# Kernel tuning notes

Hardware: AMD Instinct MI355X
Metric: run time of the kernel (lower is better)

The kernel has to match this reference:

```python
import jax, jax.numpy as jnp
import numpy as np
import math

B, N, D, H, L, F, K = 4, 256, 768, 32, 12, 3072, 128
HD = D // H
ATOM_TYPES = 64
EDGE_TYPES = ATOM_TYPES * ATOM_TYPES
BLOCKS = 1
SQRT_2PI = math.sqrt(2.0 * math.pi)


def _ln(x, g, b):
    m = jnp.mean(x, -1, keepdims=True)
    v = jnp.mean((x - m) ** 2, -1, keepdims=True)
    return (x - m) * jax.lax.rsqrt(v + 1e-5) * g + b


def _gelu(x):
    return jax.nn.gelu(x, approximate=False)


def setup_inputs():
    key = jax.random.key(0)
    ks = iter(jax.random.split(key, 64))
    def nrm(shape, s=0.02):
        return jax.random.normal(next(ks), shape, jnp.float32) * s
    inp = dict(
        atoms=jax.random.randint(next(ks), (B, N), 0, ATOM_TYPES),
        tags=jax.random.randint(next(ks), (B, N), 0, 3),
        pos=jax.random.normal(next(ks), (B, N, 3), jnp.float32) * 3.0,
        real_mask=jnp.ones((B, N), dtype=bool),
        atom_emb=nrm((ATOM_TYPES, D)),
        tag_emb=nrm((3, D)),
        gbf_means=jax.random.uniform(next(ks), (K,), jnp.float32, 0.0, 3.0),
        gbf_stds=jax.random.uniform(next(ks), (K,), jnp.float32, 0.0, 3.0),
        gbf_mul=jnp.ones((EDGE_TYPES, 1), jnp.float32),
        gbf_bias=jnp.zeros((EDGE_TYPES, 1), jnp.float32),
        bp_w1=nrm((K, K)), bp_b1=jnp.zeros((K,), jnp.float32),
        bp_w2=nrm((H, K)), bp_b2=jnp.zeros((H,), jnp.float32),
        ep_w=nrm((D, K)), ep_b=jnp.zeros((D,), jnp.float32),
        ln1_g=jnp.ones((L, D), jnp.float32), ln1_b=jnp.zeros((L, D), jnp.float32),
        wqkv=nrm((L, 3 * D, D)), bqkv=jnp.zeros((L, 3 * D), jnp.float32),
        wo=nrm((L, D, D)), bo=jnp.zeros((L, D), jnp.float32),
        ln2_g=jnp.ones((L, D), jnp.float32), ln2_b=jnp.zeros((L, D), jnp.float32),
        w1=nrm((L, F, D)), b1=jnp.zeros((L, F), jnp.float32),
        w2=nrm((L, D, F)), b2=jnp.zeros((L, D), jnp.float32),
        fln_g=jnp.ones((D,), jnp.float32), fln_b=jnp.zeros((D,), jnp.float32),
        en_w1=nrm((D, D)), en_b1=jnp.zeros((D,), jnp.float32),
        en_w2=nrm((1, D)), en_b2=jnp.zeros((1,), jnp.float32),
        eagg=nrm((3, 1), 0.01),
        nq_w=nrm((D, D)), nq_b=jnp.zeros((D,), jnp.float32),
        nk_w=nrm((D, D)), nk_b=jnp.zeros((D,), jnp.float32),
        nv_w=nrm((D, D)), nv_b=jnp.zeros((D,), jnp.float32),
        f1_w=nrm((1, D)), f1_b=jnp.zeros((1,), jnp.float32),
        f2_w=nrm((1, D)), f2_b=jnp.zeros((1,), jnp.float32),
        f3_w=nrm((1, D)), f3_b=jnp.zeros((1,), jnp.float32),
    )
    return inp


def _forward(atoms, tags, real_mask, pos, atom_emb, tag_emb, gbf_means, gbf_stds, gbf_mul, gbf_bias,
             bp_w1, bp_b1, bp_w2, bp_b2, ep_w, ep_b,
             ln1_g, ln1_b, wqkv, bqkv, wo, bo, ln2_g, ln2_b, w1, b1, w2, b2,
             fln_g, fln_b, en_w1, en_b1, en_w2, en_b2, eagg,
             nq_w, nq_b, nk_w, nk_b, nv_w, nv_b, f1_w, f1_b, f2_w, f2_b, f3_w, f3_b):
    pad = atoms == 0                                              # [B,N]
    # delta[b,i,j] = pos[b,j] - pos[b,i]  (matches pos.unsqueeze(1) - pos.unsqueeze(2))
    delta = pos[:, None, :, :] - pos[:, :, None, :]               # [B,N,N,3]
    sq = jnp.sum(delta * delta, axis=-1)
    dist = jnp.sqrt(jnp.maximum(sq, 1e-24))                       # safe norm, zero grad on diagonal
    delta = delta / (dist[..., None] + 1e-5)
    edge_type = atoms[:, :, None] * ATOM_TYPES + atoms[:, None, :]  # [B,N,N]
    # Gaussian basis layer
    mul = gbf_mul[edge_type]                                      # [B,N,N,1]
    add = gbf_bias[edge_type]                                     # [B,N,N,1]
    x = mul * dist[..., None] + add                               # [B,N,N,1] -> broadcast to K
    std = jnp.abs(gbf_stds) + 1e-5                                # [K]
    z = (x - gbf_means) / std
    gbf = jnp.exp(-0.5 * z * z) / (SQRT_2PI * std)                # [B,N,N,K]
    edge_feat = jnp.where(pad[:, None, :, None], 0.0, gbf)
    node = tag_emb[tags] + atom_emb[atoms] + (edge_feat.sum(-2) @ ep_w.T + ep_b)  # [B,N,D]
    bias = _gelu(gbf @ bp_w1.T + bp_b1) @ bp_w2.T + bp_b2         # [B,N,N,H]
    bias = jnp.transpose(bias, (0, 3, 1, 2))                      # [B,H,N,N]
    bias = jnp.where(pad[:, None, None, :], -jnp.inf, bias)
    scale = HD ** -0.5
    h = node
    for _ in range(BLOCKS):
        for l in range(L):
            r = h
            y = _ln(h, ln1_g[l], ln1_b[l])
            qkv = y @ wqkv[l].T + bqkv[l]
            q, k, v = jnp.split(qkv, 3, axis=-1)
            q = q.reshape(B, N, H, HD).transpose(0, 2, 1, 3) * scale
            k = k.reshape(B, N, H, HD).transpose(0, 2, 1, 3)
            v = v.reshape(B, N, H, HD).transpose(0, 2, 1, 3)
            a = jnp.einsum('bhid,bhjd->bhij', q, k) + bias
            a = jax.nn.softmax(a, axis=-1)
            o = jnp.einsum('bhij,bhjd->bhid', a, v).transpose(0, 2, 1, 3).reshape(B, N, D)
            h = r + (o @ wo[l].T + bo[l])
            r = h
            y = _ln(h, ln2_g[l], ln2_b[l])
            y = _gelu(y @ w1[l].T + b1[l]) @ w2[l].T + b2[l]
            h = r + y
    out = _ln(h, fln_g, fln_b)                                    # [B,N,D]
    # energy head (eval: no dropout)
    eng = _gelu(out @ en_w1.T + en_b1) @ en_w2.T + en_b2          # [B,N,1]
    eng = (eng * eagg[tags])[..., 0]                              # [B,N]
    omask = (tags > 0) & real_mask
    eng_output = (eng * omask).sum(-1)                            # [B]
    # node task head
    q = (out @ nq_w.T + nq_b).reshape(B, N, H, HD).transpose(0, 2, 1, 3) * scale
    k = (out @ nk_w.T + nk_b).reshape(B, N, H, HD).transpose(0, 2, 1, 3)
    v = (out @ nv_w.T + nv_b).reshape(B, N, H, HD).transpose(0, 2, 1, 3)
    a = jnp.einsum('bhid,bhjd->bhij', q, k) + bias
    a = jax.nn.softmax(a, axis=-1)                                # [B,H,N,N]
    # rot_attn_probs @ v, fused: [b,h,i,j]*[b,i,j,c]*[b,h,j,d] -> [b,i,c,h,d]
    xf = jnp.einsum('bhij,bijc,bhjd->bichd', a, delta, v).reshape(B, N, 3, D)
    f1 = xf[:, :, 0] @ f1_w.T + f1_b
    f2 = xf[:, :, 1] @ f2_w.T + f2_b
    f3 = xf[:, :, 2] @ f3_w.T + f3_b
    node_output = jnp.concatenate([f1, f2, f3], axis=-1)          # [B,N,3]
    return eng_output, node_output, omask[..., None]


def reference(atoms, tags, pos, real_mask, atom_emb, tag_emb, gbf_means, gbf_stds, gbf_mul, gbf_bias,
              bp_w1, bp_b1, bp_w2, bp_b2, ep_w, ep_b,
              ln1_g, ln1_b, wqkv, bqkv, wo, bo, ln2_g, ln2_b, w1, b1, w2, b2,
              fln_g, fln_b, en_w1, en_b1, en_w2, en_b2, eagg,
              nq_w, nq_b, nk_w, nk_b, nv_w, nv_b, f1_w, f1_b, f2_w, f2_b, f3_w, f3_b):
    return _forward(atoms, tags, real_mask, pos, atom_emb, tag_emb, gbf_means, gbf_stds, gbf_mul, gbf_bias,
                    bp_w1, bp_b1, bp_w2, bp_b2, ep_w, ep_b,
                    ln1_g, ln1_b, wqkv, bqkv, wo, bo, ln2_g, ln2_b, w1, b1, w2, b2,
                    fln_g, fln_b, en_w1, en_b1, en_w2, en_b2, eagg,
                    nq_w, nq_b, nk_w, nk_b, nv_w, nv_b, f1_w, f1_b, f2_w, f2_b, f3_w, f3_b)
```

## Files before the change

kernel.cpp:

```cpp
#include <hip/hip_runtime.h>
#include <math.h>

constexpr int B_ = 4, N_ = 256, D_ = 768, H_ = 32, HD_ = 24, L_ = 12, F_ = 3072, K_ = 128;
constexpr float SCALE_ = 0.20412414523193150f;
constexpr float ISQRT2_ = 0.70710678118654752f;

typedef short bf16x8 __attribute__((ext_vector_type(8)));
typedef float f32x4 __attribute__((ext_vector_type(4)));
typedef unsigned short u16x4 __attribute__((ext_vector_type(4)));
typedef unsigned short u16x8 __attribute__((ext_vector_type(8)));
typedef unsigned int u32x4 __attribute__((ext_vector_type(4)));

#define DEV __device__ __forceinline__
#define MFMA16(a, b, c) __builtin_amdgcn_mfma_f32_16x16x32_bf16(a, b, c, 0, 0, 0)

DEV void gload_lds16(const unsigned short* g, unsigned short* l) {
  __builtin_amdgcn_global_load_lds(
      (const __attribute__((address_space(1))) unsigned int*)(g),
      (__attribute__((address_space(3))) unsigned int*)(l), 16, 0, 0);
}

DEV float gelu_f(float x) { return 0.5f * x * (1.0f + erff(x * ISQRT2_)); }

DEV unsigned short f2bf(float f) {
  unsigned u = __float_as_uint(f);
  return (unsigned short)((u + 0x7FFFu + ((u >> 16) & 1u)) >> 16);
}
DEV float bf2f(unsigned short u) { return __uint_as_float(((unsigned)u) << 16); }
DEV unsigned packbf(float a, float b) {
  return (unsigned)f2bf(a) | ((unsigned)f2bf(b) << 16);
}
DEV bf16x8 u4_to_bf8(u32x4 x) { union { u32x4 a; bf16x8 b; } u; u.a = x; return u.b; }

DEV float breduce_sum(float v, float* sred, int tid) {
#pragma unroll
  for (int o = 32; o > 0; o >>= 1) v += __shfl_xor(v, o);
  if ((tid & 63) == 0) sred[tid >> 6] = v;
  __syncthreads();
  v = (sred[0] + sred[1]) + (sred[2] + sred[3]);
  __syncthreads();
  return v;
}

__global__ __launch_bounds__(256) void cast_bias_kernel(
    const float* __restrict__ w1f, const float* __restrict__ w2f,
    unsigned short* __restrict__ d1, unsigned short* __restrict__ d2) {
  const int i = blockIdx.x * 256 + threadIdx.x;
  const float* s;
  unsigned short* d;
  int j;
  if (i < 4096) { s = w1f; d = d1; j = i; }
  else { s = w2f; d = d2; j = i - 4096; }
  const float4 v = ((const float4*)s)[j];
  u16x4 o = {f2bf(v.x), f2bf(v.y), f2bf(v.z), f2bf(v.w)};
  ((u16x4*)d)[j] = o;
}

__global__ __launch_bounds__(256) void castlayer_kernel(
    const float* __restrict__ wqkv, const float* __restrict__ wo,
    const float* __restrict__ w1, const float* __restrict__ w2,
    unsigned short* __restrict__ arena) {
  const unsigned i = blockIdx.x * 256 + threadIdx.x;
  const float* s; unsigned j;
  if (i < 221184u) { s = wqkv; j = i; }
  else if (i < 294912u) { s = wo; j = i - 221184u; }
  else if (i < 589824u) { s = w1; j = i - 294912u; }
  else { s = w2; j = i - 589824u; }
  const float4 a = ((const float4*)s)[2u * j];
  const float4 b = ((const float4*)s)[2u * j + 1u];
  u16x8 o = {f2bf(a.x), f2bf(a.y), f2bf(a.z), f2bf(a.w),
             f2bf(b.x), f2bf(b.y), f2bf(b.z), f2bf(b.w)};
  ((u16x8*)arena)[i] = o;
}

__global__ __launch_bounds__(256) void castheads_kernel(
    const float* __restrict__ a, const float* __restrict__ b,
    const float* __restrict__ c, const float* __restrict__ d,
    unsigned short* __restrict__ arena) {
  const unsigned i = blockIdx.x * 256 + threadIdx.x;
  const unsigned r = i / 73728u;
  const unsigned j = i - r * 73728u;
  const float* s = (r == 0) ? a : (r == 1) ? b : (r == 2) ? c : d;
  const float4 a0 = ((const float4*)s)[2u * j];
  const float4 a1 = ((const float4*)s)[2u * j + 1u];
  u16x8 o = {f2bf(a0.x), f2bf(a0.y), f2bf(a0.z), f2bf(a0.w),
             f2bf(a1.x), f2bf(a1.y), f2bf(a1.z), f2bf(a1.w)};
  ((u16x8*)arena)[i] = o;
}

__global__ __launch_bounds__(256) void edge_pre_kernel(
    const int* __restrict__ atoms, const float* __restrict__ pos,
    const float* __restrict__ gbf_mul, const float* __restrict__ gbf_bias,
    const float* __restrict__ gbf_means, const float* __restrict__ gbf_stds,
    float* __restrict__ deltaw, float* __restrict__ xvalw, float* __restrict__ nsumw)
{
  const int tid = threadIdx.x;
  const int bi = blockIdx.x;
  const int b = bi >> 8;
  __shared__ float spos[3];
  __shared__ float sxv[256];
  __shared__ int   spad[256];
  __shared__ float red[256];
  if (tid < 3) spos[tid] = pos[(size_t)bi * 3 + tid];
  __syncthreads();
  {
    const int j = tid;
    const float px = pos[(size_t)(b * N_ + j) * 3 + 0];
    const float py = pos[(size_t)(b * N_ + j) * 3 + 1];
    const float pz = pos[(size_t)(b * N_ + j) * 3 + 2];
    const float dx = px - spos[0], dy = py - spos[1], dz = pz - spos[2];
    const float sq = dx * dx + dy * dy + dz * dz;
    const float dist = sqrtf(fmaxf(sq, 1e-24f));
    const float inv = 1.f / (dist + 1e-5f);
    const size_t e = (size_t)bi * N_ + j;
    deltaw[e * 3 + 0] = dx * inv;
    deltaw[e * 3 + 1] = dy * inv;
    deltaw[e * 3 + 2] = dz * inv;
    const int et = atoms[bi] * 64 + atoms[b * N_ + j];
    const float xv = gbf_mul[et] * dist + gbf_bias[et];
    xvalw[e] = xv;
    sxv[j] = xv;
    spad[j] = (atoms[b * N_ + j] == 0);
  }
  __syncthreads();
  const int k = tid & 127;
  const float mean = gbf_means[k];
  const float st = fabsf(gbf_stds[k]) + 1e-5f;
  const float istd = 1.f / st;
  const float coef = 0.39894228040143268f * istd;
  float acc = 0.f;
  const int jbase = tid >> 7;
  for (int t = 0; t < 128; ++t) {
    const int j = jbase + (t << 1);
    if (!spad[j]) {
      const float z = (sxv[j] - mean) * istd;
      acc += __expf(-0.5f * z * z) * coef;
    }
  }
  red[tid] = acc;
  __syncthreads();
  if (tid < 128) nsumw[(size_t)bi * K_ + tid] = red[tid] + red[tid + 128];
}

__global__ __launch_bounds__(256) void bias_mfma_kernel(
    const float* __restrict__ xvalw, const int* __restrict__ atoms,
    const float* __restrict__ gbf_means, const float* __restrict__ gbf_stds,
    const unsigned short* __restrict__ w1b, const float* __restrict__ b1,
    const unsigned short* __restrict__ w2b, const float* __restrict__ b2,
    unsigned short* __restrict__ biasb)
{
  __shared__ __align__(16) unsigned short sw1[128 * 128];
  __shared__ __align__(16) unsigned short sw2[32 * 128];
  __shared__ float smean[128], sistd[128], scoef[128], sb1[128], sb2[32];
  const int tid = threadIdx.x;
  const int l = tid & 63;
  const int w = tid >> 6;
  const size_t e0 = (size_t)blockIdx.x * 64;
  const int bB = (int)(e0 >> 16);
  const int iI = (int)((e0 >> 8) & 255);
  const int j0 = (int)(e0 & 255);
  const int lr = l & 15;
  const int lg = l >> 4;

  {
    const int rin = l >> 4;
    const int slot = l & 15;
#pragma unroll
    for (int q = 0; q < 8; ++q) {
      const int rbase = w * 32 + q * 4;
      const int row = rbase + rin;
      const int gs = slot ^ (row & 15);
      gload_lds16(w1b + row * 128 + gs * 8, &sw1[rbase * 128]);
    }
#pragma unroll
    for (int q = 0; q < 2; ++q) {
      const int rbase = w * 8 + q * 4;
      const int row = rbase + rin;
      const int gs = slot ^ (row & 15);
      gload_lds16(w2b + row * 128 + gs * 8, &sw2[rbase * 128]);
    }
  }
  if (tid < 128) {
    const float st = fabsf(gbf_stds[tid]) + 1e-5f;
    const float is = 1.f / st;
    smean[tid] = gbf_means[tid];
    sistd[tid] = is;
    scoef[tid] = 0.39894228040143268f * is;
    sb1[tid] = b1[tid];
  } else if (tid < 160) {
    sb2[tid - 128] = b2[tid - 128];
  }
  const int el = w * 16 + lr;
  const float xv = xvalw[e0 + el];
  const bool padq = (atoms[bB * N_ + j0 + el] == 0);
  __syncthreads();

  bf16x8 bG[4];
#pragma unroll
  for (int ks = 0; ks < 4; ++ks) {
    u16x8 t;
#pragma unroll
    for (int j = 0; j < 8; ++j) {
      const int k = ks * 32 + lg * 8 + j;
      const float z = (xv - smean[k]) * sistd[k];
      t[j] = f2bf(__expf(-0.5f * z * z) * scoef[k]);
    }
    union { u16x8 a; bf16x8 b; } u; u.a = t;
    bG[ks] = u.b;
  }

  f32x4 accM[8];
#pragma unroll
  for (int f = 0; f < 8; ++f) accM[f] = (f32x4)0.f;
#pragma unroll
  for (int ks = 0; ks < 4; ++ks) {
#pragma unroll
    for (int f = 0; f < 8; ++f) {
      const int row = f * 16 + lr;
      const int sl = (ks * 4 + lg) ^ (row & 15);
      const bf16x8 aW = *(const bf16x8*)&sw1[row * 128 + (sl << 3)];
      accM[f] = MFMA16(aW, bG[ks], accM[f]);
    }
  }

  unsigned pm[8][2];
#pragma unroll
  for (int f = 0; f < 8; ++f) {
    float g[4];
#pragma unroll
    for (int r = 0; r < 4; ++r)
      g[r] = gelu_f(accM[f][r] + sb1[f * 16 + lg * 4 + r]);
    pm[f][0] = packbf(g[0], g[1]);
    pm[f][1] = packbf(g[2], g[3]);
  }

  f32x4 accH[2];
  accH[0] = (f32x4)0.f; accH[1] = (f32x4)0.f;
#pragma unroll
  for (int ks = 0; ks < 4; ++ks) {
    const int s0 = ((((lg << 1)) & 3) << 4) + lr;
    const int s1 = ((((lg << 1) + 1) & 3) << 4) + lr;
    const int sel = lg >> 1;
    const unsigned a0 = __shfl(pm[2 * ks][0], s0), b0 = __shfl(pm[2 * ks + 1][0], s0);
    const unsigned a1 = __shfl(pm[2 * ks][1], s0), b1v = __shfl(pm[2 * ks + 1][1], s0);
    const unsigned a2 = __shfl(pm[2 * ks][0], s1), b2v = __shfl(pm[2 * ks + 1][0], s1);
    const unsigned a3 = __shfl(pm[2 * ks][1], s1), b3v = __shfl(pm[2 * ks + 1][1], s1);
    u32x4 bw;
    bw.x = sel ? b0 : a0;
    bw.y = sel ? b1v : a1;
    bw.z = sel ? b2v : a2;
    bw.w = sel ? b3v : a3;
    const bf16x8 bMid = u4_to_bf8(bw);
#pragma unroll
    for (int hf = 0; hf < 2; ++hf) {
      const int row = hf * 16 + lr;
      const int sl = (ks * 4 + lg) ^ (row & 15);
      const bf16x8 aW2 = *(const bf16x8*)&sw2[row * 128 + (sl << 3)];
      accH[hf] = MFMA16(aW2, bMid, accH[hf]);
    }
  }

  const size_t obase = (((size_t)bB * H_) * N_ + iI) * N_ + j0 + el;
#pragma unroll
  for (int hf = 0; hf < 2; ++hf) {
#pragma unroll
    for (int r = 0; r < 4; ++r) {
      const int h = hf * 16 + lg * 4 + r;
      const unsigned short v = padq ? (unsigned short)0xFF80
                                    : f2bf(accH[hf][r] + sb2[h]);
      biasb[obase + (size_t)h * N_ * N_] = v;
    }
  }
}

__global__ __launch_bounds__(256) void node_init_kernel(
    const int* __restrict__ atoms, const int* __restrict__ tags,
    const float* __restrict__ atom_emb, const float* __restrict__ tag_emb,
    const float* __restrict__ nsumw, const float* __restrict__ ep_w,
    const float* __restrict__ ep_b, float* __restrict__ hbuf)
{
  const int bi = blockIdx.x;
  const int tid = threadIdx.x;
  __shared__ float ns[K_];
  if (tid < K_) ns[tid] = nsumw[(size_t)bi * K_ + tid];
  __syncthreads();
  const int at = atoms[bi], tg = tags[bi];
  for (int d = tid; d < D_; d += 256) {
    float acc = tag_emb[tg * D_ + d] + atom_emb[at * D_ + d] + ep_b[d];
    const float* w = ep_w + (size_t)d * K_;
#pragma unroll 8
    for (int kk = 0; kk < K_; ++kk) acc = fmaf(ns[kk], w[kk], acc);
    hbuf[(size_t)bi * D_ + d] = acc;
  }
}

__global__ __launch_bounds__(256) void ln_kernel(
    const float* __restrict__ x, const float* __restrict__ gg,
    const float* __restrict__ bb, unsigned short* __restrict__ y)
{
  const int bi = blockIdx.x;
  const int tid = threadIdx.x;
  __shared__ float sred[4];
  const float* row = x + (size_t)bi * D_;
  const float v0 = row[tid], v1 = row[tid + 256], v2 = row[tid + 512];
  float s = breduce_sum(v0 + v1 + v2, sred, tid);
  const float mean = s * (1.f / 768.f);
  const float d0 = v0 - mean, d1 = v1 - mean, d2 = v2 - mean;
  float q = breduce_sum(d0 * d0 + d1 * d1 + d2 * d2, sred, tid);
  const float inv = rsqrtf(q * (1.f / 768.f) + 1e-5f);
  unsigned short* out = y + (size_t)bi * D_;
  out[tid]       = f2bf(d0 * inv * gg[tid]       + bb[tid]);
  out[tid + 256] = f2bf(d1 * inv * gg[tid + 256] + bb[tid + 256]);
  out[tid + 512] = f2bf(d2 * inv * gg[tid + 512] + bb[tid + 512]);
}

template <int S>
__global__ __launch_bounds__(256) void reduce_ln_kernel(
    const float* __restrict__ P, const float* __restrict__ bias,
    float* __restrict__ hbuf, const float* __restrict__ gg,
    const float* __restrict__ bb, unsigned short* __restrict__ y)
{
  const int row = blockIdx.x;
  const int tid = threadIdx.x;
  __shared__ float sred[4];
  float h[3];
#pragma unroll
  for (int t = 0; t < 3; ++t) {
    const int c = tid + (t << 8);
    float s = bias[c];
#pragma unroll
    for (int z = 0; z < S; ++z)
      s += P[((size_t)z * (B_ * N_) + row) * 768 + c];
    const float hv = hbuf[(size_t)row * 768 + c] + s;
    hbuf[(size_t)row * 768 + c] = hv;
    h[t] = hv;
  }
  float sm = breduce_sum(h[0] + h[1] + h[2], sred, tid);
  const float mean = sm * (1.f / 768.f);
  const float d0 = h[0] - mean, d1 = h[1] - mean, d2 = h[2] - mean;
  float q = breduce_sum(d0 * d0 + d1 * d1 + d2 * d2, sred, tid);
  const float inv = rsqrtf(q * (1.f / 768.f) + 1e-5f);
  unsigned short* out = y + (size_t)row * 768;
  out[tid]       = f2bf(d0 * inv * gg[tid]       + bb[tid]);
  out[tid + 256] = f2bf(d1 * inv * gg[tid + 256] + bb[tid + 256]);
  out[tid + 512] = f2bf(d2 * inv * gg[tid + 512] + bb[tid + 512]);
}

template <int EPI, int OB>
__global__ __launch_bounds__(256) void gemm_mfma(
    const unsigned short* __restrict__ A, const unsigned short* __restrict__ W,
    const float* __restrict__ bias, const float* __restrict__ bias2,
    const float* __restrict__ bias3, const float* __restrict__ bias4,
    float* __restrict__ C, unsigned short* __restrict__ Cb,
    int M, int N, int K, int lda, int ldw)
{
  if (EPI == 4) {
    const int z = blockIdx.z;
    A += (size_t)z * K;
    W += (size_t)z * K;
    C += (size_t)z * M * N;
  }
  __shared__ __align__(16) unsigned short sA[2][64 * 64];
  __shared__ __align__(16) unsigned short sB[2][64 * 64];
  const int tid = threadIdx.x;
  const int l = tid & 63;
  const int w = tid >> 6;
  const int m0 = blockIdx.y * 64;
  const int n0 = blockIdx.x * 64;
  const int wm = w >> 1, wn = w & 1;
  const int lr = l & 15;
  const int lg = l >> 4;
  const int r0 = (w << 4) + (l >> 3);
  const int s0 = (l & 7) ^ (r0 & 7);

  f32x4 acc[2][2];
#pragma unroll
  for (int mi = 0; mi < 2; ++mi)
#pragma unroll
    for (int ni = 0; ni < 2; ++ni) acc[mi][ni] = (f32x4)0.f;

  auto stage = [&](int buf, int t) {
    const size_t kb = (size_t)t << 6;
    unsigned short* lA = &sA[buf][(w << 4) << 6];
    unsigned short* lB = &sB[buf][(w << 4) << 6];
    gload_lds16(A + (size_t)(m0 + r0) * lda + kb + (s0 << 3), lA);
    gload_lds16(A + (size_t)(m0 + r0 + 8) * lda + kb + (s0 << 3), lA + 8 * 64);
    gload_lds16(W + (size_t)(n0 + r0) * ldw + kb + (s0 << 3), lB);
    gload_lds16(W + (size_t)(n0 + r0 + 8) * ldw + kb + (s0 << 3), lB + 8 * 64);
  };

  stage(0, 0);
  const int nt = K >> 6;
  for (int t = 0; t < nt; ++t) {
    __syncthreads();
    if (t + 1 < nt) stage((t + 1) & 1, t + 1);
    const unsigned short* bA = sA[t & 1];
    const unsigned short* bBs = sB[t & 1];
    bf16x8 af[2][2], bfr[2][2];
#pragma unroll
    for (int mi = 0; mi < 2; ++mi) {
      const int row = (wm << 5) + (mi << 4) + lr;
#pragma unroll
      for (int kk = 0; kk < 2; ++kk) {
        const int sl = ((kk << 2) + lg) ^ (row & 7);
        af[mi][kk] = *(const bf16x8*)&bA[(row << 6) + (sl << 3)];
      }
    }
#pragma unroll
    for (int ni = 0; ni < 2; ++ni) {
      const int row = (wn << 5) + (ni << 4) + lr;
#pragma unroll
      for (int kk = 0; kk < 2; ++kk) {
        const int sl = ((kk << 2) + lg) ^ (row & 7);
        bfr[ni][kk] = *(const bf16x8*)&bBs[(row << 6) + (sl << 3)];
      }
    }
#pragma unroll
    for (int kk = 0; kk < 2; ++kk)
#pragma unroll
      for (int mi = 0; mi < 2; ++mi)
#pragma unroll
        for (int ni = 0; ni < 2; ++ni)
          acc[mi][ni] = MFMA16(af[mi][kk], bfr[ni][kk], acc[mi][ni]);
  }

#pragma unroll
  for (int mi = 0; mi < 2; ++mi)
#pragma unroll
    for (int ni = 0; ni < 2; ++ni) {
      const int n = n0 + (wn << 5) + (ni << 4) + lr;
      float bv = 0.f;
      int seg = 0;
      if (EPI == 3) {
        seg = n / 768;
        const float* bp = (seg == 0) ? bias : (seg == 1) ? bias2
                         : (seg == 2) ? bias3 : bias4;
        bv = bp[n - seg * 768];
      } else if (EPI != 4) {
        bv = bias[n];
      }
#pragma unroll
      for (int r = 0; r < 4; ++r) {
        const int m = m0 + (wm << 5) + (mi << 4) + lg * 4 + r;
        float v = acc[mi][ni][r] + bv;
        if (EPI == 1) v = gelu_f(v);
        if (EPI == 3 && seg == 3) v = gelu_f(v);
        if (OB) Cb[(size_t)m * N + n] = f2bf(v);
        else C[(size_t)m * N + n] = v;
      }
    }
}

template <bool PROBS>
__global__ __launch_bounds__(256) void attn_mfma_kernel(
    const unsigned short* __restrict__ Q, const unsigned short* __restrict__ Kp,
    const unsigned short* __restrict__ Vp, const int stride,
    const unsigned short* __restrict__ biasb, unsigned short* __restrict__ obuf,
    unsigned short* __restrict__ aprob,
    const float* __restrict__ f1w, const float* __restrict__ f2w,
    const float* __restrict__ f3w, float* __restrict__ wv)
{
  __shared__ __align__(16) unsigned short sK[256 * 40];
  __shared__ __align__(16) unsigned short sVt[32 * 264];
  __shared__ __align__(16) unsigned short sP[64 * 264];
  const int tid = threadIdx.x;
  const int l = tid & 63, w = tid >> 6;
  const int bh = blockIdx.x, b = bh >> 5, hh = bh & 31;
  const int i0 = blockIdx.y * 64;
  const int lr = l & 15, lg = l >> 4;

#pragma unroll
  for (int it = 0; it < 3; ++it) {
    const int c = tid + (it << 8);
    const int row = c / 3, part = c - row * 3;
    *(u16x8*)&sK[row * 40 + part * 8] =
        *(const u16x8*)&Kp[(size_t)(b * N_ + row) * stride + hh * HD_ + part * 8];
  }
  {
    u16x8 z = {0, 0, 0, 0, 0, 0, 0, 0};
    *(u16x8*)&sK[tid * 40 + 24] = z;
  }
  if (!PROBS) {
    const int j = tid;
    const unsigned short* vr = &Vp[(size_t)(b * N_ + j) * stride + hh * HD_];
    const u16x8 v0 = *(const u16x8*)vr;
    const u16x8 v1 = *(const u16x8*)(vr + 8);
    const u16x8 v2 = *(const u16x8*)(vr + 16);
#pragma unroll
    for (int d = 0; d < 8; ++d) {
      sVt[d * 264 + j] = v0[d];
      sVt[(8 + d) * 264 + j] = v1[d];
      sVt[(16 + d) * 264 + j] = v2[d];
    }
  }
  bf16x8 aQ;
  if (lg < 3) {
    const u16x8 q = *(const u16x8*)&Q[(size_t)(b * N_ + i0 + (w << 4) + lr) * stride + hh * HD_ + lg * 8];
    union { u16x8 a; bf16x8 b; } u; u.a = q;
    aQ = u.b;
  } else {
    bf16x8 t = {0, 0, 0, 0, 0, 0, 0, 0};
    aQ = t;
  }
  __syncthreads();

  f32x4 acc[16];
#pragma unroll
  for (int ni = 0; ni < 16; ++ni) {
    const bf16x8 bK = *(const bf16x8*)&sK[(ni * 16 + lr) * 40 + lg * 8];
    acc[ni] = MFMA16(aQ, bK, (f32x4)0.f);
  }

  float invr[4];
#pragma unroll
  for (int r = 0; r < 4; ++r) {
    const int iloc = (w << 4) + lg * 4 + r;
    const unsigned short* bp =
        &biasb[(((size_t)(b * H_ + hh)) * N_ + i0 + iloc) * N_ + lr];
    float mx = -INFINITY;
#pragma unroll
    for (int ni = 0; ni < 16; ++ni) {
      const float s = acc[ni][r] * SCALE_ + bf2f(bp[ni * 16]);
      acc[ni][r] = s;
      mx = fmaxf(mx, s);
    }
    mx = fmaxf(mx, __shfl_xor(mx, 1));
    mx = fmaxf(mx, __shfl_xor(mx, 2));
    mx = fmaxf(mx, __shfl_xor(mx, 4));
    mx = fmaxf(mx, __shfl_xor(mx, 8));
    float sum = 0.f;
#pragma unroll
    for (int ni = 0; ni < 16; ++ni) {
      const float e = __expf(acc[ni][r] - mx);
      acc[ni][r] = e;
      sum += e;
    }
    sum += __shfl_xor(sum, 1);
    sum += __shfl_xor(sum, 2);
    sum += __shfl_xor(sum, 4);
    sum += __shfl_xor(sum, 8);
    const float inv = 1.f / sum;
    invr[r] = inv;
#pragma unroll
    for (int ni = 0; ni < 16; ++ni)
      sP[iloc * 264 + ni * 16 + lr] = f2bf(PROBS ? acc[ni][r] * inv
                                                 : acc[ni][r]);
  }
  __syncthreads();

  if (PROBS) {
#pragma unroll
    for (int it = 0; it < 8; ++it) {
      const int idx = tid + it * 256;
      const int row = idx >> 5, c = idx & 31;
      *(u16x8*)&aprob[(((size_t)(b * H_ + hh)) * N_ + i0 + row) * N_ + c * 8] =
          *(const u16x8*)&sP[row * 264 + c * 8];
    }
    if (blockIdx.y == 0) {
      const int j = tid;
      const unsigned short* vr = &Vp[(size_t)(b * N_ + j) * stride + hh * HD_];
      const u16x8 v0 = *(const u16x8*)vr;
      const u16x8 v1 = *(const u16x8*)(vr + 8);
      const u16x8 v2 = *(const u16x8*)(vr + 16);
      float s0 = 0.f, s1 = 0.f, s2 = 0.f;
#pragma unroll
      for (int d = 0; d < 8; ++d) {
        const float e0 = bf2f(v0[d]), e1 = bf2f(v1[d]), e2 = bf2f(v2[d]);
        s0 = fmaf(e0, f1w[hh * HD_ + d], s0);
        s0 = fmaf(e1, f1w[hh * HD_ + 8 + d], s0);
        s0 = fmaf(e2, f1w[hh * HD_ + 16 + d], s0);
        s1 = fmaf(e0, f2w[hh * HD_ + d], s1);
        s1 = fmaf(e1, f2w[hh * HD_ + 8 + d], s1);
        s1 = fmaf(e2, f2w[hh * HD_ + 16 + d], s1);
        s2 = fmaf(e0, f3w[hh * HD_ + d], s2);
        s2 = fmaf(e1, f3w[hh * HD_ + 8 + d], s2);
        s2 = fmaf(e2, f3w[hh * HD_ + 16 + d], s2);
      }
      wv[((size_t)(0 * B_ + b) * H_ + hh) * N_ + j] = s0;
      wv[((size_t)(1 * B_ + b) * H_ + hh) * N_ + j] = s1;
      wv[((size_t)(2 * B_ + b) * H_ + hh) * N_ + j] = s2;
    }
  } else {
    f32x4 accO[2];
    accO[0] = (f32x4)0.f; accO[1] = (f32x4)0.f;
#pragma unroll
    for (int ks = 0; ks < 8; ++ks) {
      const bf16x8 aP = *(const bf16x8*)&sP[((w << 4) + lr) * 264 + ks * 32 + lg * 8];
      const bf16x8 bV0 = *(const bf16x8*)&sVt[lr * 264 + ks * 32 + lg * 8];
      const bf16x8 bV1 = *(const bf16x8*)&sVt[(16 + lr) * 264 + ks * 32 + lg * 8];
      accO[0] = MFMA16(aP, bV0, accO[0]);
      accO[1] = MFMA16(aP, bV1, accO[1]);
    }
#pragma unroll
    for (int ni = 0; ni < 2; ++ni) {
      const int n = ni * 16 + lr;
      if (n < HD_) {
#pragma unroll
        for (int r = 0; r < 4; ++r) {
          const int i = i0 + (w << 4) + lg * 4 + r;
          obuf[(size_t)(b * N_ + i) * D_ + hh * HD_ + n] = f2bf(accO[ni][r] * invr[r]);
        }
      }
    }
  }
}

__global__ __launch_bounds__(256) void engnode_kernel(
    const unsigned short* __restrict__ t1, const int stride,
    const float* __restrict__ en_w2, const float* __restrict__ en_b2,
    const float* __restrict__ eagg, const int* __restrict__ tags,
    float* __restrict__ engpn)
{
  const int bi = blockIdx.x;
  const int tid = threadIdx.x;
  __shared__ float sred[4];
  const unsigned short* row = t1 + (size_t)bi * stride;
  float acc = bf2f(row[tid]) * en_w2[tid] + bf2f(row[tid + 256]) * en_w2[tid + 256] +
              bf2f(row[tid + 512]) * en_w2[tid + 512];
  acc = breduce_sum(acc, sred, tid);
  if (tid == 0) {
    const int tg = tags[bi];
    engpn[bi] = (tg > 0) ? (acc + en_b2[0]) * eagg[tg] : 0.f;
  }
}

__global__ __launch_bounds__(256) void engsum_omask_kernel(
    const float* __restrict__ engpn, const int* __restrict__ tags,
    float* __restrict__ out)
{
  const int bid = blockIdx.x;
  const int tid = threadIdx.x;
  if (bid < 4) {
    __shared__ float sred[4];
    float v = breduce_sum(engpn[bid * N_ + tid], sred, tid);
    if (tid == 0) out[bid] = v;
  } else {
    const int idx = (bid - 4) * 256 + tid;
    out[4 + B_ * N_ * 3 + idx] = (tags[idx] > 0) ? 1.f : 0.f;
  }
}

__global__ __launch_bounds__(256) void nodeout_kernel(
    const unsigned short* __restrict__ aprob, const float* __restrict__ wv,
    const float* __restrict__ deltaw, const float* __restrict__ f1b,
    const float* __restrict__ f2b, const float* __restrict__ f3b,
    float* __restrict__ out)
{
  const int bi = blockIdx.x;
  const int tid = threadIdx.x;
  const int b = bi >> 8;
  const int i = bi & 255;
  __shared__ float sred[4];
  const unsigned short* ap = aprob + (((size_t)b * H_) * N_ + i) * N_ + tid;
  const float* wv0 = wv + ((size_t)(0 * B_ + b) * H_) * N_ + tid;
  const float* wv1 = wv + ((size_t)(1 * B_ + b) * H_) * N_ + tid;
  const float* wv2 = wv + ((size_t)(2 * B_ + b) * H_) * N_ + tid;
  float s0 = 0.f, s1 = 0.f, s2 = 0.f;
  for (int hh = 0; hh < H_; ++hh) {
    const float p = bf2f(ap[(size_t)hh * N_ * N_]);
    s0 = fmaf(p, wv0[(size_t)hh * N_], s0);
    s1 = fmaf(p, wv1[(size_t)hh * N_], s1);
    s2 = fmaf(p, wv2[(size_t)hh * N_], s2);
  }
  const float* dl = &deltaw[((size_t)bi * N_ + tid) * 3];
  s0 *= dl[0];
  s1 *= dl[1];
  s2 *= dl[2];
  s0 = breduce_sum(s0, sred, tid);
  s1 = breduce_sum(s1, sred, tid);
  s2 = breduce_sum(s2, sred, tid);
  if (tid == 0) {
    out[4 + bi * 3 + 0] = s0 + f1b[0];
    out[4 + bi * 3 + 1] = s1 + f2b[0];
    out[4 + bi * 3 + 2] = s2 + f3b[0];
  }
}

extern "C" void kernel_launch(void* const* d_in, const int* in_sizes, int n_in,
                              void* d_out, int out_size, void* d_ws, size_t ws_size,
                              hipStream_t stream) {
  (void)in_sizes; (void)n_in; (void)out_size; (void)ws_size;
  const int*   atoms     = (const int*)  d_in[0];
  const int*   tags      = (const int*)  d_in[1];
  const float* pos       = (const float*)d_in[2];
  const float* atom_emb  = (const float*)d_in[4];
  const float* tag_emb   = (const float*)d_in[5];
  const float* gbf_means = (const float*)d_in[6];
  const float* gbf_stds  = (const float*)d_in[7];
  const float* gbf_mul   = (const float*)d_in[8];
  const float* gbf_bias  = (const float*)d_in[9];
  const float* bp_w1     = (const float*)d_in[10];
  const float* bp_b1     = (const float*)d_in[11];
  const float* bp_w2     = (const float*)d_in[12];
  const float* bp_b2     = (const float*)d_in[13];
  const float* ep_w      = (const float*)d_in[14];
  const float* ep_b      = (const float*)d_in[15];
  const float* ln1_g     = (const float*)d_in[16];
  const float* ln1_b     = (const float*)d_in[17];
  const float* wqkv      = (const float*)d_in[18];
  const float* bqkv      = (const float*)d_in[19];
  const float* wo        = (const float*)d_in[20];
  const float* bo        = (const float*)d_in[21];
  const float* ln2_g     = (const float*)d_in[22];
  const float* ln2_b     = (const float*)d_in[23];
  const float* w1        = (const float*)d_in[24];
  const float* b1        = (const float*)d_in[25];
  const float* w2        = (const float*)d_in[26];
  const float* b2        = (const float*)d_in[27];
  const float* fln_g     = (const float*)d_in[28];
  const float* fln_b     = (const float*)d_in[29];
  const float* en_w1     = (const float*)d_in[30];
  const float* en_b1     = (const float*)d_in[31];
  const float* en_w2     = (const float*)d_in[32];
  const float* en_b2     = (const float*)d_in[33];
  const float* eagg      = (const float*)d_in[34];
  const float* nq_w      = (const float*)d_in[35];
  const float* nq_b      = (const float*)d_in[36];
  const float* nk_w      = (const float*)d_in[37];
  const float* nk_b      = (const float*)d_in[38];
  const float* nv_w      = (const float*)d_in[39];
  const float* nv_b      = (const float*)d_in[40];
  const float* f1_w      = (const float*)d_in[41];
  const float* f1_b      = (const float*)d_in[42];
  const float* f2_w      = (const float*)d_in[43];
  const float* f2_b      = (const float*)d_in[44];
  const float* f3_w      = (const float*)d_in[45];
  const float* f3_b      = (const float*)d_in[46];

  char* wsB = (char*)d_ws;
  size_t off = 0;
  auto alloc = [&](size_t bytes) {
    void* p = wsB + off;
    off = (off + bytes + 255) & ~(size_t)255;
    return p;
  };
  unsigned short* biasb   = (unsigned short*)alloc((size_t)B_ * H_ * N_ * N_ * 2);
  unsigned short* aprobb  = (unsigned short*)alloc((size_t)B_ * H_ * N_ * N_ * 2);
  float*          deltaw  = (float*)alloc((size_t)B_ * N_ * N_ * 3 * 4);
  float*          xvalw   = (float*)alloc((size_t)B_ * N_ * N_ * 4);
  float*          nsumw   = (float*)alloc((size_t)B_ * N_ * K_ * 4);
  float*          hbuf    = (float*)alloc((size_t)B_ * N_ * D_ * 4);
  unsigned short* qkvb    = (unsigned short*)alloc((size_t)B_ * N_ * 3 * D_ * 2);
  unsigned short* qn4b    = (unsigned short*)alloc((size_t)B_ * N_ * 3072 * 2);
  unsigned short* ybf     = (unsigned short*)alloc((size_t)B_ * N_ * D_ * 2);
  unsigned short* obf     = (unsigned short*)alloc((size_t)B_ * N_ * D_ * 2);
  unsigned short* midbf   = (unsigned short*)alloc((size_t)B_ * N_ * F_ * 2);
  unsigned short* outbf   = (unsigned short*)alloc((size_t)B_ * N_ * D_ * 2);
  unsigned short* arena   = (unsigned short*)alloc((size_t)7077888 * 2);
  unsigned short* headsb  = (unsigned short*)alloc((size_t)2359296 * 2);
  unsigned short* bw1b    = (unsigned short*)alloc((size_t)K_ * K_ * 2);
  unsigned short* bw2b    = (unsigned short*)alloc((size_t)H_ * K_ * 2);
  float*          wopart  = (float*)alloc((size_t)2 * B_ * N_ * D_ * 4);
  float*          ffpart  = (float*)alloc((size_t)4 * B_ * N_ * D_ * 4);
  float*          wvb     = (float*)alloc((size_t)3 * B_ * H_ * N_ * 4);
  float*          engpn   = (float*)alloc((size_t)B_ * N_ * 4);

  const int BN = B_ * N_;
  float* outp = (float*)d_out;
  const size_t OQKV = 0, OWO = 1769472, OW1 = 2359296, OW2 = 4718592;

  edge_pre_kernel<<<BN, 256, 0, stream>>>(atoms, pos, gbf_mul, gbf_bias,
                                          gbf_means, gbf_stds, deltaw, xvalw, nsumw);
  cast_bias_kernel<<<20, 256, 0, stream>>>(bp_w1, bp_w2, bw1b, bw2b);
  bias_mfma_kernel<<<B_ * N_ * N_ / 64, 256, 0, stream>>>(
      xvalw, atoms, gbf_means, gbf_stds, bw1b, bp_b1, bw2b, bp_b2, biasb);
  node_init_kernel<<<BN, 256, 0, stream>>>(atoms, tags, atom_emb, tag_emb,
                                           nsumw, ep_w, ep_b, hbuf);
  ln_kernel<<<BN, 256, 0, stream>>>(hbuf, ln1_g, ln1_b, ybf);

  for (int l = 0; l < L_; ++l) {
    castlayer_kernel<<<3456, 256, 0, stream>>>(
        wqkv + (size_t)l * 3 * D_ * D_, wo + (size_t)l * D_ * D_,
        w1 + (size_t)l * F_ * D_, w2 + (size_t)l * D_ * F_, arena);
    gemm_mfma<0, 1><<<dim3(36, 16), 256, 0, stream>>>(
        ybf, arena + OQKV, bqkv + (size_t)l * 3 * D_, nullptr, nullptr, nullptr,
        nullptr, qkvb, BN, 3 * D_, D_, D_, D_);
    attn_mfma_kernel<false><<<dim3(B_ * H_, 4), 256, 0, stream>>>(
        qkvb, qkvb + D_, qkvb + 2 * D_, 3 * D_, biasb, obf, nullptr,
        nullptr, nullptr, nullptr, nullptr);
    gemm_mfma<4, 0><<<dim3(12, 16, 2), 256, 0, stream>>>(
        obf, arena + OWO, nullptr, nullptr, nullptr, nullptr,
        wopart, nullptr, BN, D_, 384, D_, D_);
    reduce_ln_kernel<2><<<BN, 256, 0, stream>>>(
        wopart, bo + (size_t)l * D_, hbuf, ln2_g + (size_t)l * D_,
        ln2_b + (size_t)l * D_, ybf);
    gemm_mfma<1, 1><<<dim3(48, 16), 256, 0, stream>>>(
        ybf, arena + OW1, b1 + (size_t)l * F_, nullptr, nullptr, nullptr,
        nullptr, midbf, BN, F_, D_, D_, D_);
    gemm_mfma<4, 0><<<dim3(12, 16, 4), 256, 0, stream>>>(
        midbf, arena + OW2, nullptr, nullptr, nullptr, nullptr,
        ffpart, nullptr, BN, D_, 768, F_, F_);
    const bool last = (l == L_ - 1);
    reduce_ln_kernel<4><<<BN, 256, 0, stream>>>(
        ffpart, b2 + (size_t)l * D_, hbuf,
        last ? fln_g : ln1_g + (size_t)(l + 1) * D_,
        last ? fln_b : ln1_b + (size_t)(l + 1) * D_,
        last ? outbf : ybf);
  }

  castheads_kernel<<<1152, 256, 0, stream>>>(nq_w, nk_w, nv_w, en_w1, headsb);

  gemm_mfma<3, 1><<<dim3(48, 16), 256, 0, stream>>>(
      outbf, headsb, nq_b, nk_b, nv_b, en_b1,
      nullptr, qn4b, BN, 3072, D_, D_, D_);

  attn_mfma_kernel<true><<<dim3(B_ * H_, 4), 256, 0, stream>>>(
      qn4b, qn4b + 768, qn4b + 1536, 3072, biasb, nullptr, aprobb,
      f1_w, f2_w, f3_w, wvb);
  nodeout_kernel<<<BN, 256, 0, stream>>>(aprobb, wvb, deltaw,
                                         f1_b, f2_b, f3_b, outp);

  engnode_kernel<<<BN, 256, 0, stream>>>(qn4b + 2304, 3072, en_w2, en_b2,
                                         eagg, tags, engpn);
  engsum_omask_kernel<<<8, 256, 0, stream>>>(engpn, tags, outp);
}
```

Measured before the change: 1.015 ms.

## Fuse next-layer weight cast into reduce_ln with double-buffered arena

The per-layer bf16 weight cast kernel, and the final head-weight cast, are folded into the reduce_ln_kernel that follows the Wo GEMM as extra blocks. Each one casts the next layer's weights into the other half of a double-buffered arena. This removes separate kernel launches and lets the memory-bound cast run alongside the LayerNorm rows. In exchange the arena doubles in size, and the LN kernel gains extra parameters and a branch.

```diff
diff --git a/kernel.cpp b/kernel.cpp
--- a/kernel.cpp
+++ b/kernel.cpp
@@ -70,21 +70,6 @@
   const float4 b = ((const float4*)s)[2u * j + 1u];
   u16x8 o = {f2bf(a.x), f2bf(a.y), f2bf(a.z), f2bf(a.w),
              f2bf(b.x), f2bf(b.y), f2bf(b.z), f2bf(b.w)};
-  ((u16x8*)arena)[i] = o;
-}
-
-__global__ __launch_bounds__(256) void castheads_kernel(
-    const float* __restrict__ a, const float* __restrict__ b,
-    const float* __restrict__ c, const float* __restrict__ d,
-    unsigned short* __restrict__ arena) {
-  const unsigned i = blockIdx.x * 256 + threadIdx.x;
-  const unsigned r = i / 73728u;
-  const unsigned j = i - r * 73728u;
-  const float* s = (r == 0) ? a : (r == 1) ? b : (r == 2) ? c : d;
-  const float4 a0 = ((const float4*)s)[2u * j];
-  const float4 a1 = ((const float4*)s)[2u * j + 1u];
-  u16x8 o = {f2bf(a0.x), f2bf(a0.y), f2bf(a0.z), f2bf(a0.w),
-             f2bf(a1.x), f2bf(a1.y), f2bf(a1.z), f2bf(a1.w)};
   ((u16x8*)arena)[i] = o;
 }
 
@@ -318,10 +303,34 @@
 __global__ __launch_bounds__(256) void reduce_ln_kernel(
     const float* __restrict__ P, const float* __restrict__ bias,
     float* __restrict__ hbuf, const float* __restrict__ gg,
-    const float* __restrict__ bb, unsigned short* __restrict__ y)
-{
+    const float* __restrict__ bb, unsigned short* __restrict__ y,
+    const float* __restrict__ c0, const float* __restrict__ c1,
+    const float* __restrict__ c2, const float* __restrict__ c3,
+    unsigned short* __restrict__ cdst, int mode)
+{
+  const int tid = threadIdx.x;
+  if (blockIdx.x >= B_ * N_) {
+    const unsigned ci = (blockIdx.x - B_ * N_) * 256u + tid;
+    const float* s;
+    unsigned j;
+    if (mode == 1) {
+      if (ci < 221184u) { s = c0; j = ci; }
+      else if (ci < 294912u) { s = c1; j = ci - 221184u; }
+      else if (ci < 589824u) { s = c2; j = ci - 294912u; }
+      else { s = c3; j = ci - 589824u; }
+    } else {
+      const unsigned r = ci / 73728u;
+      j = ci - r * 73728u;
+      s = (r == 0) ? c0 : (r == 1) ? c1 : (r == 2) ? c2 : c3;
+    }
+    const float4 a = ((const float4*)s)[2u * j];
+    const float4 b = ((const float4*)s)[2u * j + 1u];
+    u16x8 o = {f2bf(a.x), f2bf(a.y), f2bf(a.z), f2bf(a.w),
+               f2bf(b.x), f2bf(b.y), f2bf(b.z), f2bf(b.w)};
+    ((u16x8*)cdst)[ci] = o;
+    return;
+  }
   const int row = blockIdx.x;
-  const int tid = threadIdx.x;
   __shared__ float sred[4];
   float h[3];
 #pragma unroll
@@ -746,7 +755,7 @@
   unsigned short* obf     = (unsigned short*)alloc((size_t)B_ * N_ * D_ * 2);
   unsigned short* midbf   = (unsigned short*)alloc((size_t)B_ * N_ * F_ * 2);
   unsigned short* outbf   = (unsigned short*)alloc((size_t)B_ * N_ * D_ * 2);
-  unsigned short* arena   = (unsigned short*)alloc((size_t)7077888 * 2);
+  unsigned short* arena   = (unsigned short*)alloc((size_t)2 * 7077888 * 2);
   unsigned short* headsb  = (unsigned short*)alloc((size_t)2359296 * 2);
   unsigned short* bw1b    = (unsigned short*)alloc((size_t)K_ * K_ * 2);
   unsigned short* bw2b    = (unsigned short*)alloc((size_t)H_ * K_ * 2);
@@ -757,6 +766,7 @@
 
   const int BN = B_ * N_;
   float* outp = (float*)d_out;
+  const size_t AR = 7077888;
   const size_t OQKV = 0, OWO = 1769472, OW1 = 2359296, OW2 = 4718592;
 
   edge_pre_kernel<<<BN, 256, 0, stream>>>(atoms, pos, gbf_mul, gbf_bias,
@@ -767,38 +777,48 @@
   node_init_kernel<<<BN, 256, 0, stream>>>(atoms, tags, atom_emb, tag_emb,
                                            nsumw, ep_w, ep_b, hbuf);
   ln_kernel<<<BN, 256, 0, stream>>>(hbuf, ln1_g, ln1_b, ybf);
+  castlayer_kernel<<<3456, 256, 0, stream>>>(
+      wqkv, wo, w1, w2, arena);
 
   for (int l = 0; l < L_; ++l) {
-    castlayer_kernel<<<3456, 256, 0, stream>>>(
-        wqkv + (size_t)l * 3 * D_ * D_, wo + (size_t)l * D_ * D_,
-        w1 + (size_t)l * F_ * D_, w2 + (size_t)l * D_ * F_, arena);
+    unsigned short* ar = arena + (size_t)(l & 1) * AR;
     gemm_mfma<0, 1><<<dim3(36, 16), 256, 0, stream>>>(
-        ybf, arena + OQKV, bqkv + (size_t)l * 3 * D_, nullptr, nullptr, nullptr,
+        ybf, ar + OQKV, bqkv + (size_t)l * 3 * D_, nullptr, nullptr, nullptr,
         nullptr, qkvb, BN, 3 * D_, D_, D_, D_);
     attn_mfma_kernel<false><<<dim3(B_ * H_, 4), 256, 0, stream>>>(
         qkvb, qkvb + D_, qkvb + 2 * D_, 3 * D_, biasb, obf, nullptr,
         nullptr, nullptr, nullptr, nullptr);
     gemm_mfma<4, 0><<<dim3(12, 16, 2), 256, 0, stream>>>(
-        obf, arena + OWO, nullptr, nullptr, nullptr, nullptr,
+        obf, ar + OWO, nullptr, nullptr, nullptr, nullptr,
         wopart, nullptr, BN, D_, 384, D_, D_);
-    reduce_ln_kernel<2><<<BN, 256, 0, stream>>>(
-        wopart, bo + (size_t)l * D_, hbuf, ln2_g + (size_t)l * D_,
-        ln2_b + (size_t)l * D_, ybf);
+    if (l + 1 < L_) {
+      const int lc = l + 1;
+      reduce_ln_kernel<2><<<BN + 3456, 256, 0, stream>>>(
+          wopart, bo + (size_t)l * D_, hbuf, ln2_g + (size_t)l * D_,
+          ln2_b + (size_t)l * D_, ybf,
+          wqkv + (size_t)lc * 3 * D_ * D_, wo + (size_t)lc * D_ * D_,
+          w1 + (size_t)lc * F_ * D_, w2 + (size_t)lc * D_ * F_,
+          arena + (size_t)(lc & 1) * AR, 1);
+    } else {
+      reduce_ln_kernel<2><<<BN + 1152, 256, 0, stream>>>(
+          wopart, bo + (size_t)l * D_, hbuf, ln2_g + (size_t)l * D_,
+          ln2_b + (size_t)l * D_, ybf,
+          nq_w, nk_w, nv_w, en_w1, headsb, 2);
+    }
     gemm_mfma<1, 1><<<dim3(48, 16), 256, 0, stream>>>(
-        ybf, arena + OW1, b1 + (size_t)l * F_, nullptr, nullptr, nullptr,
+        ybf, ar + OW1, b1 + (size_t)l * F_, nullptr, nullptr, nullptr,
         nullptr, midbf, BN, F_, D_, D_, D_);
     gemm_mfma<4, 0><<<dim3(12, 16, 4), 256, 0, stream>>>(
-        midbf, arena + OW2, nullptr, nullptr, nullptr, nullptr,
+        midbf, ar + OW2, nullptr, nullptr, nullptr, nullptr,
         ffpart, nullptr, BN, D_, 768, F_, F_);
     const bool last = (l == L_ - 1);
     reduce_ln_kernel<4><<<BN, 256, 0, stream>>>(
         ffpart, b2 + (size_t)l * D_, hbuf,
         last ? fln_g : ln1_g + (size_t)(l + 1) * D_,
         last ? fln_b : ln1_b + (size_t)(l + 1) * D_,
-        last ? outbf : ybf);
-  }
-
-  castheads_kernel<<<1152, 256, 0, stream>>>(nq_w, nk_w, nv_w, en_w1, headsb);
+        last ? outbf : ybf,
+        nullptr, nullptr, nullptr, nullptr, nullptr, 0);
+  }
 
   gemm_mfma<3, 1><<<dim3(48, 16), 256, 0, stream>>>(
       outbf, headsb, nq_b, nk_b, nv_b, en_b1,
```

Result: faster. 987.6 us (-2.7%).
